# Performance work log

Hardware: AMD Instinct MI355X
Metric: run time of the kernel (lower is better)

Reference implementation:

```python
import jax, jax.numpy as jnp
import numpy as np

DIM = 64        # feature channels of x
HEADS = 4
POS_DIM = 3
NUM_IDS = 8
STR_IN = 512    # strength_linear input size
B, S, W = 4, 1024, 8   # batch, sequence (S1), source-views (S2)


def setup_inputs() -> dict:
    key = jax.random.key(0)
    ks = jax.random.split(key, 18)
    stdv = 1.0 / np.sqrt(DIM * DIM)  # embedding init per module
    d8 = DIM // 8
    u = lambda k, shp, s: jax.random.uniform(k, shp, jnp.float32, -s, s)
    return {
        "x": jax.random.normal(ks[0], (B, DIM, S, W), jnp.float32),
        "pos": jax.random.normal(ks[1], (B, S, POS_DIM), jnp.float32),
        "strength": jax.random.normal(ks[2], (STR_IN,), jnp.float32),
        "embed_id1": 3,
        "q_emb_w": u(ks[3], (NUM_IDS, DIM * DIM), stdv),
        "k_emb_w": u(ks[4], (NUM_IDS, DIM * DIM), stdv),
        "v_emb_w": u(ks[5], (NUM_IDS, DIM * DIM), stdv),
        "pos_w1": u(ks[6], (POS_DIM, POS_DIM), 1.0 / np.sqrt(POS_DIM)),
        "pos_b1": u(ks[7], (POS_DIM,), 1.0 / np.sqrt(POS_DIM)),
        "pos_w2": u(ks[8], (d8, POS_DIM), 1.0 / np.sqrt(POS_DIM)),
        "pos_b2": u(ks[9], (d8,), 1.0 / np.sqrt(POS_DIM)),
        "head_w": u(ks[10], (HEADS, d8), 1.0 / np.sqrt(d8)),
        "head_b": u(ks[11], (HEADS,), 1.0 / np.sqrt(d8)),
        "gate": jnp.ones((HEADS,), jnp.float32),
        "out_w": u(ks[12], (DIM, DIM), 1.0 / np.sqrt(DIM)),
        "out_b": u(ks[13], (DIM,), 1.0 / np.sqrt(DIM)),
        "str_w": u(ks[14], (DIM, STR_IN), 1.0 / np.sqrt(STR_IN)),
        "str_b": u(ks[15], (DIM,), 1.0 / np.sqrt(STR_IN)),
    }


def reference(x, pos, strength, embed_id1, q_emb_w, k_emb_w, v_emb_w,
              pos_w1, pos_b1, pos_w2, pos_b2, head_w, head_b, gate,
              out_w, out_b, str_w, str_b):
    # strength projection: Linear(512, dim)
    s = strength @ str_w.T + str_b                    # [dim]
    xt = jnp.transpose(x, (0, 2, 3, 1))               # [B, S, W, dim]
    qe = q_emb_w[embed_id1].reshape(DIM, DIM)
    ke = k_emb_w[embed_id1].reshape(DIM, DIM)
    ve = v_emb_w[embed_id1].reshape(DIM, DIM)

    def proj(emb):
        y = xt @ emb.T + s                            # [B, S, W, dim]
        # collapse (W, dim) -> (heads, head_dim), heads to axis 1
        y = y.reshape(B, S, HEADS, -1)
        return jnp.transpose(y, (0, 2, 1, 3))         # [B, H, S, hd]

    q, k, v = proj(qe), proj(ke), proj(ve)
    hd = q.shape[-1]
    attn = jax.nn.softmax(jnp.einsum("bhsd,bhtd->bhst", q, k) / np.sqrt(hd), axis=-1)

    # relative-position attention branch
    ph = jax.nn.relu(pos @ pos_w1.T + pos_b1) @ pos_w2.T + pos_b2   # [B, S, dim//8]
    diff = ph[:, :, None, :] - ph[:, None, :, :]                    # [B, S, S, dim//8]
    pos_attn = jnp.transpose(diff @ head_w.T + head_b, (0, 3, 1, 2))
    pos_attn = jax.nn.softmax(pos_attn, axis=-1)                    # [B, H, S, S]

    g = jax.nn.sigmoid(gate).reshape(1, -1, 1, 1)
    attn = (1.0 - g) * attn + g * pos_attn
    attn = attn / jnp.sum(attn, axis=-1, keepdims=True)

    out = jnp.einsum("bhst,bhtd->bhsd", attn, v)      # [B, H, S, hd]
    out = jnp.transpose(out, (0, 2, 1, 3)).reshape(B, S, W, DIM)
    return out @ out_w.T + out_b                      # [B, S, W, dim]
```

## Files before the change

kernel.cpp:

```cpp
#include <hip/hip_runtime.h>
#include <math.h>
#include <stdint.h>

#define B_ 4
#define S_ 1024
#define F_ 512
#define HD 128
#define SOFT_C 4.0f

typedef __attribute__((ext_vector_type(8))) short short8;
typedef __attribute__((ext_vector_type(4))) float f32x4;
typedef __attribute__((ext_vector_type(4))) unsigned int u32x4;
typedef __attribute__((ext_vector_type(2))) unsigned int u32x2;

__device__ __forceinline__ unsigned short f2bf(float f) {
    unsigned int u = __float_as_uint(f);
    u = (u + 0x7FFFu + ((u >> 16) & 1u)) >> 16;
    return (unsigned short)u;
}
__device__ __forceinline__ float bf2f(unsigned int s) {
    return __uint_as_float(s << 16);
}
__device__ __forceinline__ void pack_hilo(const float* v, u32x4& hi, u32x4& lo) {
    #pragma unroll
    for (int p = 0; p < 4; ++p) {
        unsigned int h0 = f2bf(v[2 * p]), h1 = f2bf(v[2 * p + 1]);
        float l0 = v[2 * p] - bf2f(h0), l1 = v[2 * p + 1] - bf2f(h1);
        hi[p] = h0 | (h1 << 16);
        lo[p] = (unsigned int)f2bf(l0) | ((unsigned int)f2bf(l1) << 16);
    }
}

__global__ __launch_bounds__(256) void k_qkv(
    const float* __restrict__ x, const int* __restrict__ embed_id,
    const float* __restrict__ qw, const float* __restrict__ kw,
    const float* __restrict__ vw,
    const float* __restrict__ strength, const float* __restrict__ str_w,
    const float* __restrict__ str_b,
    const float* __restrict__ pos, const float* __restrict__ pw1,
    const float* __restrict__ pb1, const float* __restrict__ pw2,
    const float* __restrict__ pb2, const float* __restrict__ head_w,
    unsigned short* __restrict__ yqh, unsigned short* __restrict__ ykh,
    unsigned short* __restrict__ yvt2,
    float* __restrict__ sv_g, float* __restrict__ xbar)
{
    __shared__ unsigned short whi[3][4096];
    __shared__ unsigned short wlo[3][4096];
    __shared__ float part_s[4][64];
    __shared__ float sv_s[64], svq_s[64];
    __shared__ float xr_s[4][8];
    __shared__ float red_s[4][4];
    __shared__ float inv_s[4];

    const int tid  = threadIdx.x;
    const int wv   = tid >> 6;
    const int lane = tid & 63;
    const int quad = lane >> 4;
    const int l15  = lane & 15;
    const float SCALE = 0.08838834764831845f;

    if (blockIdx.x >= 256) {
        const int bi = blockIdx.x - 256;
        const int b = bi >> 6, c = bi & 63;
        float w1_[9], b1_[3], w2_[24], b2_[8], hw_[32];
        #pragma unroll
        for (int i = 0; i < 9; ++i)  w1_[i] = pw1[i];
        #pragma unroll
        for (int i = 0; i < 3; ++i)  b1_[i] = pb1[i];
        #pragma unroll
        for (int i = 0; i < 24; ++i) w2_[i] = pw2[i];
        #pragma unroll
        for (int i = 0; i < 8; ++i)  b2_[i] = pb2[i];
        #pragma unroll
        for (int i = 0; i < 32; ++i) hw_[i] = head_w[i];

        float pv_[4][4];
        float ps[4] = {0.f, 0.f, 0.f, 0.f};
        #pragma unroll
        for (int rr = 0; rr < 4; ++rr) {
            const int s = tid * 4 + rr;
            float p0 = pos[(b * S_ + s) * 3 + 0];
            float p1 = pos[(b * S_ + s) * 3 + 1];
            float p2 = pos[(b * S_ + s) * 3 + 2];
            float h0 = fmaxf(0.f, p0 * w1_[0] + p1 * w1_[1] + p2 * w1_[2] + b1_[0]);
            float h1 = fmaxf(0.f, p0 * w1_[3] + p1 * w1_[4] + p2 * w1_[5] + b1_[1]);
            float h2 = fmaxf(0.f, p0 * w1_[6] + p1 * w1_[7] + p2 * w1_[8] + b1_[2]);
            float ph[8];
            #pragma unroll
            for (int o8 = 0; o8 < 8; ++o8)
                ph[o8] = h0 * w2_[o8 * 3] + h1 * w2_[o8 * 3 + 1]
                       + h2 * w2_[o8 * 3 + 2] + b2_[o8];
            #pragma unroll
            for (int h = 0; h < 4; ++h) {
                float A = 0.f;
                #pragma unroll
                for (int o8 = 0; o8 < 8; ++o8) A += ph[o8] * hw_[h * 8 + o8];
                pv_[rr][h] = __expf(-A - 1.0f);
                ps[h] += pv_[rr][h];
            }
        }
        #pragma unroll
        for (int h = 0; h < 4; ++h)
            #pragma unroll
            for (int off = 1; off < 64; off <<= 1)
                ps[h] += __shfl_xor(ps[h], off);
        if (lane == 0)
            #pragma unroll
            for (int h = 0; h < 4; ++h) red_s[wv][h] = ps[h];
        __syncthreads();
        if (tid < 4)
            inv_s[tid] = 1.f / (red_s[0][tid] + red_s[1][tid]
                              + red_s[2][tid] + red_s[3][tid]);
        __syncthreads();

        const float* xc = x + (size_t)b * 524288 + c * 8192;
        float acc[8] = {};
        #pragma unroll
        for (int rr = 0; rr < 4; ++rr) {
            const int s = tid * 4 + rr;
            f32x4 x0 = *(const f32x4*)(xc + s * 8);
            f32x4 x1 = *(const f32x4*)(xc + s * 8 + 4);
            float q0 = pv_[rr][0] * inv_s[0];
            float q1 = pv_[rr][1] * inv_s[1];
            float q2 = pv_[rr][2] * inv_s[2];
            float q3 = pv_[rr][3] * inv_s[3];
            acc[0] += q0 * x0[0]; acc[1] += q0 * x0[1];
            acc[2] += q1 * x0[2]; acc[3] += q1 * x0[3];
            acc[4] += q2 * x1[0]; acc[5] += q2 * x1[1];
            acc[6] += q3 * x1[2]; acc[7] += q3 * x1[3];
        }
        #pragma unroll
        for (int j = 0; j < 8; ++j)
            #pragma unroll
            for (int off = 1; off < 64; off <<= 1)
                acc[j] += __shfl_xor(acc[j], off);
        if (lane == 0)
            #pragma unroll
            for (int j = 0; j < 8; ++j) xr_s[wv][j] = acc[j];
        __syncthreads();
        if (tid < 8)
            xbar[(b * 8 + tid) * 64 + c] = xr_s[0][tid] + xr_s[1][tid]
                                         + xr_s[2][tid] + xr_s[3][tid];
        return;
    }

    const int id = embed_id[0];

    for (int cc = tid; cc < 1536; cc += 256) {
        const int m  = cc >> 9;
        const int e0 = (cc & 511) << 3;
        const float* src = (m == 0 ? qw : m == 1 ? kw : vw) + id * 4096 + e0;
        const float sc = (m == 0) ? SCALE : 1.0f;
        f32x4 a0 = *(const f32x4*)src;
        f32x4 a1 = *(const f32x4*)(src + 4);
        float v8[8] = {a0[0] * sc, a0[1] * sc, a0[2] * sc, a0[3] * sc,
                       a1[0] * sc, a1[1] * sc, a1[2] * sc, a1[3] * sc};
        u32x4 hi, lo;
        pack_hilo(v8, hi, lo);
        const int r = e0 >> 6, c = e0 & 63;
        const int off = ((r >> 4) * 2 + (c >> 5)) * 512
                      + ((c >> 3) & 3) * 128 + (r & 15) * 8;
        *(u32x4*)(&whi[m][off]) = hi;
        *(u32x4*)(&wlo[m][off]) = lo;
    }

    {
        const float* wrow = str_w + lane * 512 + wv * 128;
        const float* st   = strength + wv * 128;
        float a = 0.f;
        #pragma unroll
        for (int j4 = 0; j4 < 32; ++j4) {
            f32x4 wv4 = *(const f32x4*)(wrow + j4 * 4);
            f32x4 s4  = *(const f32x4*)(st + j4 * 4);
            a += wv4[0] * s4[0] + wv4[1] * s4[1] + wv4[2] * s4[2] + wv4[3] * s4[3];
        }
        part_s[wv][lane] = a;
    }
    __syncthreads();
    if (tid < 64) {
        float v = part_s[0][tid] + part_s[1][tid] + part_s[2][tid]
                + part_s[3][tid] + str_b[tid];
        sv_s[tid]  = v;
        svq_s[tid] = v * SCALE;
        if (blockIdx.x == 0) sv_g[tid] = v;
    }
    __syncthreads();

    float svq_l[4], sv_l[4];
    #pragma unroll
    for (int nt = 0; nt < 4; ++nt) {
        svq_l[nt] = svq_s[nt * 16 + l15];
        sv_l[nt]  = sv_s[nt * 16 + l15];
    }
    f32x4 svA[4];
    #pragma unroll
    for (int mt = 0; mt < 4; ++mt)
        svA[mt] = *(const f32x4*)&sv_s[mt * 16 + quad * 4];

    #pragma unroll
    for (int u = 0; u < 2; ++u) {
        const int r0   = (blockIdx.x * 2 + u) * 64 + wv * 16;
        const int b    = r0 >> 13;
        const int rloc = (r0 & 8191) + l15;
        const float* xb = x + (size_t)b * 524288;

        u32x4 xhi[2], xlo[2];
        #pragma unroll
        for (int kc = 0; kc < 2; ++kc) {
            float xv[8];
            #pragma unroll
            for (int j = 0; j < 8; ++j)
                xv[j] = xb[(kc * 32 + quad * 8 + j) * 8192 + rloc];
            pack_hilo(xv, xhi[kc], xlo[kc]);
        }

        int idxq[4];
        #pragma unroll
        for (int rr = 0; rr < 4; ++rr) {
            const int rl = quad * 4 + rr;
            const int w_ = rl & 7;
            const int s_loc = ((r0 & 8191) >> 3) + (rl >> 3);
            idxq[rr] = (b * 4 + (w_ >> 1)) * 131072 + s_loc * 128 + (w_ & 1) * 64 + l15;
        }

        const int row_g = r0 + l15;
        const int s_idx = (row_g >> 3) & 1023;
        const int w_idx = row_g & 7;
        const int bh    = b * 4 + (w_idx >> 1);
        const int dbase = (w_idx & 1) * 64;
        unsigned short* vtb = yvt2 + (size_t)bh * 131072 + (s_idx >> 6) * 8192
                            + (size_t)dbase * 64 + (s_idx & 63);

        #pragma unroll
        for (int mat = 0; mat < 2; ++mat) {
            const unsigned short* mh = whi[mat];
            const unsigned short* ml = wlo[mat];
            f32x4 acc[4] = {};
            #pragma unroll
            for (int kc = 0; kc < 2; ++kc)
                #pragma unroll
                for (int nt = 0; nt < 4; ++nt) {
                    const int off = (nt * 2 + kc) * 512 + quad * 128 + l15 * 8;
                    u32x4 ehi = *(const u32x4*)(mh + off);
                    u32x4 elo = *(const u32x4*)(ml + off);
                    acc[nt] = __builtin_amdgcn_mfma_f32_16x16x32_bf16(
                        __builtin_bit_cast(short8, xhi[kc]),
                        __builtin_bit_cast(short8, ehi), acc[nt], 0, 0, 0);
                    acc[nt] = __builtin_amdgcn_mfma_f32_16x16x32_bf16(
                        __builtin_bit_cast(short8, xlo[kc]),
                        __builtin_bit_cast(short8, ehi), acc[nt], 0, 0, 0);
                    acc[nt] = __builtin_amdgcn_mfma_f32_16x16x32_bf16(
                        __builtin_bit_cast(short8, xhi[kc]),
                        __builtin_bit_cast(short8, elo), acc[nt], 0, 0, 0);
                }
            unsigned short* y = (mat == 0 ? yqh : ykh);
            const float* svp = (mat == 0 ? svq_l : sv_l);
            #pragma unroll
            for (int nt = 0; nt < 4; ++nt)
                #pragma unroll
                for (int rr = 0; rr < 4; ++rr)
                    y[(size_t)idxq[rr] + nt * 16] = f2bf(acc[nt][rr] + svp[nt]);
        }

        {
            const unsigned short* mh = whi[2];
            const unsigned short* ml = wlo[2];
            f32x4 acc[4] = {};
            #pragma unroll
            for (int kc = 0; kc < 2; ++kc)
                #pragma unroll
                for (int mt = 0; mt < 4; ++mt) {
                    const int off = (mt * 2 + kc) * 512 + quad * 128 + l15 * 8;
                    u32x4 ehi = *(const u32x4*)(mh + off);
                    u32x4 elo = *(const u32x4*)(ml + off);
                    acc[mt] = __builtin_amdgcn_mfma_f32_16x16x32_bf16(
                        __builtin_bit_cast(short8, ehi),
                        __builtin_bit_cast(short8, xhi[kc]), acc[mt], 0, 0, 0);
                    acc[mt] = __builtin_amdgcn_mfma_f32_16x16x32_bf16(
                        __builtin_bit_cast(short8, ehi),
                        __builtin_bit_cast(short8, xlo[kc]), acc[mt], 0, 0, 0);
                    acc[mt] = __builtin_amdgcn_mfma_f32_16x16x32_bf16(
                        __builtin_bit_cast(short8, elo),
                        __builtin_bit_cast(short8, xhi[kc]), acc[mt], 0, 0, 0);
                }
            #pragma unroll
            for (int mt = 0; mt < 4; ++mt)
                #pragma unroll
                for (int rr = 0; rr < 4; ++rr) {
                    const int c = mt * 16 + quad * 4 + rr;
                    vtb[(size_t)c * 64] = f2bf(acc[mt][rr] + svA[mt][rr]);
                }
        }
    }
}

__global__ __launch_bounds__(256, 2) void k_attn(
    const unsigned short* __restrict__ yqh, const unsigned short* __restrict__ ykh,
    const unsigned short* __restrict__ yvt2,
    const float* __restrict__ xbar, const float* __restrict__ vw,
    const int* __restrict__ embed_id, const float* __restrict__ sv,
    const float* __restrict__ gate,
    const float* __restrict__ out_w, const float* __restrict__ out_b,
    float* __restrict__ out)
{
    __shared__ __align__(16) unsigned short kx[2][64 * 136];
    __shared__ __align__(16) unsigned short vx[2][128 * 72];
    __shared__ float vbar_s[128];
    __shared__ float vbarP_s[128];
    __shared__ float lsq_s[2][2][16];

    const int tid  = threadIdx.x;
    const int w    = tid >> 6;
    const int lane = tid & 63;
    const int quad = lane >> 4;
    const int l15  = lane & 15;
    const int bh = blockIdx.x & 15, qt = blockIdx.x >> 4;
    const int b = bh >> 2, h = bh & 3;
    const int s0 = qt * 32;
    const int qh = w >> 1;
    const int ts = w & 1;

    const unsigned short* ykb = ykh + (size_t)bh * 131072;
    const unsigned short* yvb = yvt2 + (size_t)bh * 131072;

    if (tid < 128) {
        const int c = tid & 63, wloc = tid >> 6;
        const float* ver = vw + embed_id[0] * 4096 + c * 64;
        const float* xbr = xbar + (b * 8 + h * 2 + wloc) * 64;
        float a = sv[c];
        #pragma unroll
        for (int j4 = 0; j4 < 16; ++j4) {
            f32x4 e4 = *(const f32x4*)(ver + j4 * 4);
            f32x4 x4 = *(const f32x4*)(xbr + j4 * 4);
            a += e4[0] * x4[0] + e4[1] * x4[1] + e4[2] * x4[2] + e4[3] * x4[3];
        }
        vbar_s[wloc * 64 + c] = a;
    }

    u32x4 qf[4];
    #pragma unroll
    for (int kc = 0; kc < 4; ++kc)
        qf[kc] = *(const u32x4*)(yqh + (size_t)bh * 131072
                 + (s0 + qh * 16 + l15) * 128 + kc * 32 + quad * 8);

    #pragma unroll
    for (int r = 0; r < 4; ++r) {
        const int off = r * 2048 + tid * 8;
        *(u32x4*)&kx[0][(off >> 7) * 136 + (off & 127)] =
            *(const u32x4*)(ykb + off);
        *(u32x4*)&vx[0][(off >> 6) * 72 + (off & 63)] =
            *(const u32x4*)(yvb + off);
    }
    __syncthreads();

    if (tid < 128) {
        const int seg = tid >> 6, dq = tid & 63;
        const float* wr = out_w + dq * 64;
        float a = 0.f;
        #pragma unroll
        for (int j4 = 0; j4 < 16; ++j4) {
            f32x4 w4 = *(const f32x4*)(wr + j4 * 4);
            f32x4 v4 = *(const f32x4*)&vbar_s[seg * 64 + j4 * 4];
            a += w4[0] * v4[0] + w4[1] * v4[1] + w4[2] * v4[2] + w4[3] * v4[3];
        }
        vbarP_s[seg * 64 + dq] = a;
    }

    f32x4 o[8] = {};
    float lsum = 0.f;
    const int srcA = ((quad & 1) << 5) + l15;

    for (int it = 0; it < 16; ++it) {
        const int cur = it & 1;
        u32x4 kst[4], vst[4];
        const bool pre = (it < 15);
        if (pre) {
            const unsigned short* ksrc = ykb + (it + 1) * 8192;
            const unsigned short* vsrc = yvb + (it + 1) * 8192;
            #pragma unroll
            for (int r = 0; r < 4; ++r)
                kst[r] = *(const u32x4*)(ksrc + r * 2048 + tid * 8);
            #pragma unroll
            for (int r = 0; r < 4; ++r)
                vst[r] = *(const u32x4*)(vsrc + r * 2048 + tid * 8);
        }

        const unsigned short* kxc = kx[cur];
        const unsigned short* vxc = vx[cur];

        f32x4 sa0 = {}, sa1 = {};
        #pragma unroll
        for (int kc = 0; kc < 4; ++kc) {
            u32x4 a0 = *(const u32x4*)&kxc[(ts * 32 + l15) * 136 + kc * 32 + quad * 8];
            sa0 = __builtin_amdgcn_mfma_f32_16x16x32_bf16(
                __builtin_bit_cast(short8, a0),
                __builtin_bit_cast(short8, qf[kc]), sa0, 0, 0, 0);
        }
        #pragma unroll
        for (int kc = 0; kc < 4; ++kc) {
            u32x4 a1 = *(const u32x4*)&kxc[(ts * 32 + 16 + l15) * 136 + kc * 32 + quad * 8];
            sa1 = __builtin_amdgcn_mfma_f32_16x16x32_bf16(
                __builtin_bit_cast(short8, a1),
                __builtin_bit_cast(short8, qf[kc]), sa1, 0, 0, 0);
        }

        float p0[4], p1[4];
        #pragma unroll
        for (int r = 0; r < 4; ++r) {
            p0[r] = __expf(sa0[r] - SOFT_C);
            p1[r] = __expf(sa1[r] - SOFT_C);
            lsum += p0[r] + p1[r];
        }

        unsigned int pk00 = (unsigned int)f2bf(p0[0]) | ((unsigned int)f2bf(p0[1]) << 16);
        unsigned int pk01 = (unsigned int)f2bf(p0[2]) | ((unsigned int)f2bf(p0[3]) << 16);
        unsigned int pk10 = (unsigned int)f2bf(p1[0]) | ((unsigned int)f2bf(p1[1]) << 16);
        unsigned int pk11 = (unsigned int)f2bf(p1[2]) | ((unsigned int)f2bf(p1[3]) << 16);
        unsigned int sel0 = (quad < 2) ? pk00 : pk10;
        unsigned int sel1 = (quad < 2) ? pk01 : pk11;
        u32x4 pf;
        pf[0] = (unsigned int)__shfl((int)sel0, srcA);
        pf[1] = (unsigned int)__shfl((int)sel1, srcA);
        pf[2] = (unsigned int)__shfl((int)sel0, srcA + 16);
        pf[3] = (unsigned int)__shfl((int)sel1, srcA + 16);

        #pragma unroll
        for (int dt = 0; dt < 8; ++dt) {
            u32x4 vf = *(const u32x4*)&vxc[(dt * 16 + l15) * 72 + ts * 32 + quad * 8];
            o[dt] = __builtin_amdgcn_mfma_f32_16x16x32_bf16(
                __builtin_bit_cast(short8, vf),
                __builtin_bit_cast(short8, pf), o[dt], 0, 0, 0);
        }

        if (pre) {
            #pragma unroll
            for (int r = 0; r < 4; ++r) {
                const int off = r * 2048 + tid * 8;
                *(u32x4*)&kx[cur ^ 1][(off >> 7) * 136 + (off & 127)] = kst[r];
            }
            #pragma unroll
            for (int r = 0; r < 4; ++r) {
                const int off = r * 2048 + tid * 8;
                *(u32x4*)&vx[cur ^ 1][(off >> 6) * 72 + (off & 63)] = vst[r];
            }
        }
        __syncthreads();
    }

    float* obuf = (float*)&kx[0][0];
    {
        float* ow_ = obuf + ((qh * 2 + ts) * 16 + l15) * 132;
        #pragma unroll
        for (int dt = 0; dt < 8; ++dt)
            *(f32x4*)(ow_ + dt * 16 + quad * 4) = o[dt];
    }
    lsum += __shfl_xor(lsum, 16);
    lsum += __shfl_xor(lsum, 32);
    if (quad == 0) lsq_s[qh][ts][l15] = lsum;
    __syncthreads();

    const float gf = 1.f / (1.f + __expf(-gate[h]));
    const float cf = (1.f - gf) / (lsq_s[qh][0][l15] + lsq_s[qh][1][l15]);
    const float* oa  = obuf + ((qh * 2 + 0) * 16 + l15) * 132;
    const float* obp = obuf + ((qh * 2 + 1) * 16 + l15) * 132;

    u32x4 bhi[2], blo[2];
    #pragma unroll
    for (int kc = 0; kc < 2; ++kc) {
        const int off = ts * 64 + kc * 32 + quad * 8;
        f32x4 a0 = *(const f32x4*)(oa + off);
        f32x4 a1 = *(const f32x4*)(oa + off + 4);
        f32x4 c0 = *(const f32x4*)(obp + off);
        f32x4 c1 = *(const f32x4*)(obp + off + 4);
        float yv[8] = {cf * (a0[0] + c0[0]), cf * (a0[1] + c0[1]),
                       cf * (a0[2] + c0[2]), cf * (a0[3] + c0[3]),
                       cf * (a1[0] + c1[0]), cf * (a1[1] + c1[1]),
                       cf * (a1[2] + c1[2]), cf * (a1[3] + c1[3])};
        pack_hilo(yv, bhi[kc], blo[kc]);
    }

    f32x4 acc[4] = {};
    #pragma unroll
    for (int kc = 0; kc < 2; ++kc)
        #pragma unroll
        for (int mt = 0; mt < 4; ++mt) {
            const float* wsrc2 = out_w + (mt * 16 + l15) * 64 + kc * 32 + quad * 8;
            f32x4 w0 = *(const f32x4*)wsrc2;
            f32x4 w1 = *(const f32x4*)(wsrc2 + 4);
            float wv8[8] = {w0[0], w0[1], w0[2], w0[3], w1[0], w1[1], w1[2], w1[3]};
            u32x4 ahi, alo;
            pack_hilo(wv8, ahi, alo);
            acc[mt] = __builtin_amdgcn_mfma_f32_16x16x32_bf16(
                __builtin_bit_cast(short8, ahi),
                __builtin_bit_cast(short8, bhi[kc]), acc[mt], 0, 0, 0);
            acc[mt] = __builtin_amdgcn_mfma_f32_16x16x32_bf16(
                __builtin_bit_cast(short8, ahi),
                __builtin_bit_cast(short8, blo[kc]), acc[mt], 0, 0, 0);
            acc[mt] = __builtin_amdgcn_mfma_f32_16x16x32_bf16(
                __builtin_bit_cast(short8, alo),
                __builtin_bit_cast(short8, bhi[kc]), acc[mt], 0, 0, 0);
        }

    const int w_seg = h * 2 + ts;
    const size_t rowb = ((size_t)(b * S_ + s0 + qh * 16 + l15) * 8 + w_seg) * 64;
    #pragma unroll
    for (int mt = 0; mt < 4; ++mt) {
        f32x4 vb   = *(const f32x4*)&vbarP_s[ts * 64 + mt * 16 + quad * 4];
        f32x4 bias = *(const f32x4*)(out_b + mt * 16 + quad * 4);
        f32x4 res;
        #pragma unroll
        for (int j = 0; j < 4; ++j) res[j] = acc[mt][j] + gf * vb[j] + bias[j];
        *(f32x4*)(out + rowb + mt * 16 + quad * 4) = res;
    }
}

extern "C" void kernel_launch(void* const* d_in, const int* in_sizes, int n_in,
                              void* d_out, int out_size, void* d_ws, size_t ws_size,
                              hipStream_t stream) {
    (void)in_sizes; (void)n_in; (void)out_size; (void)ws_size;
    const float* x        = (const float*)d_in[0];
    const float* pos      = (const float*)d_in[1];
    const float* strength = (const float*)d_in[2];
    const int*   embed_id = (const int*)d_in[3];
    const float* qw       = (const float*)d_in[4];
    const float* kw       = (const float*)d_in[5];
    const float* vw       = (const float*)d_in[6];
    const float* pw1      = (const float*)d_in[7];
    const float* pb1      = (const float*)d_in[8];
    const float* pw2      = (const float*)d_in[9];
    const float* pb2      = (const float*)d_in[10];
    const float* head_w   = (const float*)d_in[11];
    const float* gate     = (const float*)d_in[13];
    const float* out_w    = (const float*)d_in[14];
    const float* out_b    = (const float*)d_in[15];
    const float* str_w    = (const float*)d_in[16];
    const float* str_b    = (const float*)d_in[17];
    float* out = (float*)d_out;

    unsigned short* yqh   = (unsigned short*)d_ws;
    unsigned short* ykh   = yqh + 2097152;
    unsigned short* yvt2  = ykh + 2097152;
    float* sv   = (float*)(yvt2 + 2097152);
    float* xbar = sv + 64;

    k_qkv<<<512, 256, 0, stream>>>(x, embed_id, qw, kw, vw,
                                   strength, str_w, str_b,
                                   pos, pw1, pb1, pw2, pb2, head_w,
                                   yqh, ykh, yvt2, sv, xbar);
    k_attn<<<512, 256, 0, stream>>>(yqh, ykh, yvt2, xbar, vw, embed_id, sv,
                                    gate, out_w, out_b, out);
}
```

Before: 141.0 us.

## Load K/V MFMA fragments directly from global into registers, drop LDS staging

Replaces the LDS double-buffered K/V tile staging in the attention kernel with direct per-lane global loads of the MFMA operand fragments into registers, software-pipelined with two register buffers. This removes the LDS writes and reads and the per-iteration __syncthreads. In exchange, each wave fetches K/V separately, so global/L2 traffic rises and register pressure grows (32 extra u32x4 live), which may hurt occupancy under launch_bounds(256,2).

```diff
diff --git a/kernel.cpp b/kernel.cpp
--- a/kernel.cpp
+++ b/kernel.cpp
@@ -303,8 +303,7 @@
     const float* __restrict__ out_w, const float* __restrict__ out_b,
     float* __restrict__ out)
 {
-    __shared__ __align__(16) unsigned short kx[2][64 * 136];
-    __shared__ __align__(16) unsigned short vx[2][128 * 72];
+    __shared__ __align__(16) float obuf[64 * 132];
     __shared__ float vbar_s[128];
     __shared__ float vbarP_s[128];
     __shared__ float lsq_s[2][2][16];
@@ -320,8 +319,10 @@
     const int qh = w >> 1;
     const int ts = w & 1;
 
-    const unsigned short* ykb = ykh + (size_t)bh * 131072;
-    const unsigned short* yvb = yvt2 + (size_t)bh * 131072;
+    const unsigned short* kfb = ykh + (size_t)bh * 131072
+                              + (ts * 32 + l15) * 128 + quad * 8;
+    const unsigned short* vfb = yvt2 + (size_t)bh * 131072
+                              + l15 * 64 + ts * 32 + quad * 8;
 
     if (tid < 128) {
         const int c = tid & 63, wloc = tid >> 6;
@@ -343,14 +344,6 @@
         qf[kc] = *(const u32x4*)(yqh + (size_t)bh * 131072
                  + (s0 + qh * 16 + l15) * 128 + kc * 32 + quad * 8);
 
-    #pragma unroll
-    for (int r = 0; r < 4; ++r) {
-        const int off = r * 2048 + tid * 8;
-        *(u32x4*)&kx[0][(off >> 7) * 136 + (off & 127)] =
-            *(const u32x4*)(ykb + off);
-        *(u32x4*)&vx[0][(off >> 6) * 72 + (off & 63)] =
-            *(const u32x4*)(yvb + off);
-    }
     __syncthreads();
 
     if (tid < 128) {
@@ -370,39 +363,31 @@
     float lsum = 0.f;
     const int srcA = ((quad & 1) << 5) + l15;
 
-    for (int it = 0; it < 16; ++it) {
-        const int cur = it & 1;
-        u32x4 kst[4], vst[4];
-        const bool pre = (it < 15);
-        if (pre) {
-            const unsigned short* ksrc = ykb + (it + 1) * 8192;
-            const unsigned short* vsrc = yvb + (it + 1) * 8192;
-            #pragma unroll
-            for (int r = 0; r < 4; ++r)
-                kst[r] = *(const u32x4*)(ksrc + r * 2048 + tid * 8);
-            #pragma unroll
-            for (int r = 0; r < 4; ++r)
-                vst[r] = *(const u32x4*)(vsrc + r * 2048 + tid * 8);
-        }
-
-        const unsigned short* kxc = kx[cur];
-        const unsigned short* vxc = vx[cur];
-
+    auto loadkv = [&](int it, u32x4* ka, u32x4* vv) {
+        const unsigned short* kt = kfb + it * 8192;
+        #pragma unroll
+        for (int kc = 0; kc < 4; ++kc) {
+            ka[kc]     = *(const u32x4*)(kt + kc * 32);
+            ka[4 + kc] = *(const u32x4*)(kt + 2048 + kc * 32);
+        }
+        const unsigned short* vt = vfb + it * 8192;
+        #pragma unroll
+        for (int dt = 0; dt < 8; ++dt)
+            vv[dt] = *(const u32x4*)(vt + dt * 1024);
+    };
+
+    auto step = [&](const u32x4* ka, const u32x4* vv) {
         f32x4 sa0 = {}, sa1 = {};
         #pragma unroll
-        for (int kc = 0; kc < 4; ++kc) {
-            u32x4 a0 = *(const u32x4*)&kxc[(ts * 32 + l15) * 136 + kc * 32 + quad * 8];
+        for (int kc = 0; kc < 4; ++kc)
             sa0 = __builtin_amdgcn_mfma_f32_16x16x32_bf16(
-                __builtin_bit_cast(short8, a0),
+                __builtin_bit_cast(short8, ka[kc]),
                 __builtin_bit_cast(short8, qf[kc]), sa0, 0, 0, 0);
-        }
-        #pragma unroll
-        for (int kc = 0; kc < 4; ++kc) {
-            u32x4 a1 = *(const u32x4*)&kxc[(ts * 32 + 16 + l15) * 136 + kc * 32 + quad * 8];
+        #pragma unroll
+        for (int kc = 0; kc < 4; ++kc)
             sa1 = __builtin_amdgcn_mfma_f32_16x16x32_bf16(
-                __builtin_bit_cast(short8, a1),
+                __builtin_bit_cast(short8, ka[4 + kc]),
                 __builtin_bit_cast(short8, qf[kc]), sa1, 0, 0, 0);
-        }
 
         float p0[4], p1[4];
         #pragma unroll
@@ -425,29 +410,22 @@
         pf[3] = (unsigned int)__shfl((int)sel1, srcA + 16);
 
         #pragma unroll
-        for (int dt = 0; dt < 8; ++dt) {
-            u32x4 vf = *(const u32x4*)&vxc[(dt * 16 + l15) * 72 + ts * 32 + quad * 8];
+        for (int dt = 0; dt < 8; ++dt)
             o[dt] = __builtin_amdgcn_mfma_f32_16x16x32_bf16(
-                __builtin_bit_cast(short8, vf),
+                __builtin_bit_cast(short8, vv[dt]),
                 __builtin_bit_cast(short8, pf), o[dt], 0, 0, 0);
-        }
-
-        if (pre) {
-            #pragma unroll
-            for (int r = 0; r < 4; ++r) {
-                const int off = r * 2048 + tid * 8;
-                *(u32x4*)&kx[cur ^ 1][(off >> 7) * 136 + (off & 127)] = kst[r];
-            }
-            #pragma unroll
-            for (int r = 0; r < 4; ++r) {
-                const int off = r * 2048 + tid * 8;
-                *(u32x4*)&vx[cur ^ 1][(off >> 6) * 72 + (off & 63)] = vst[r];
-            }
-        }
-        __syncthreads();
-    }
-
-    float* obuf = (float*)&kx[0][0];
+    };
+
+    u32x4 kaA[8], vvA[8], kaB[8], vvB[8];
+    loadkv(0, kaA, vvA);
+    for (int it2 = 0; it2 < 8; ++it2) {
+        const int itA = it2 * 2;
+        loadkv(itA + 1, kaB, vvB);
+        step(kaA, vvA);
+        if (itA + 2 < 16) loadkv(itA + 2, kaA, vvA);
+        step(kaB, vvB);
+    }
+
     {
         float* ow_ = obuf + ((qh * 2 + ts) * 16 + l15) * 132;
         #pragma unroll
```

New measurement: 180.8 us. 1.28x slower.

## Double query tile per attention block to share K/V staging across 8 waves

Applied to the files above, without the earlier changes.

Changes k_attn to launch 256 blocks of 512 threads, each covering 64 queries in two wave groups that share one double-buffered K/V tile in shared memory. Each K/V tile is loaded once per 64 queries instead of once per 32, halving global K/V traffic and per-thread staging loads. In exchange, shared memory use grows (the output scratch buffer must now hold 8 waves' results), there are half as many blocks to spread across CUs, and barriers now synchronize 8 waves.

```diff
diff --git a/kernel.cpp b/kernel.cpp
--- a/kernel.cpp
+++ b/kernel.cpp
@@ -294,7 +294,7 @@
     }
 }
 
-__global__ __launch_bounds__(256, 2) void k_attn(
+__global__ __launch_bounds__(512, 2) void k_attn(
     const unsigned short* __restrict__ yqh, const unsigned short* __restrict__ ykh,
     const unsigned short* __restrict__ yvt2,
     const float* __restrict__ xbar, const float* __restrict__ vw,
@@ -303,11 +303,13 @@
     const float* __restrict__ out_w, const float* __restrict__ out_b,
     float* __restrict__ out)
 {
-    __shared__ __align__(16) unsigned short kx[2][64 * 136];
-    __shared__ __align__(16) unsigned short vx[2][128 * 72];
+    __shared__ __align__(16) unsigned char smem_kv[71680];
     __shared__ float vbar_s[128];
     __shared__ float vbarP_s[128];
-    __shared__ float lsq_s[2][2][16];
+    __shared__ float lsq_s[2][2][2][16];
+
+    unsigned short* kxb = (unsigned short*)smem_kv;
+    unsigned short* vxb = (unsigned short*)(smem_kv + 34816);
 
     const int tid  = threadIdx.x;
     const int w    = tid >> 6;
@@ -316,9 +318,11 @@
     const int l15  = lane & 15;
     const int bh = blockIdx.x & 15, qt = blockIdx.x >> 4;
     const int b = bh >> 2, h = bh & 3;
-    const int s0 = qt * 32;
-    const int qh = w >> 1;
-    const int ts = w & 1;
+    const int g  = w >> 2;
+    const int wl = w & 3;
+    const int qh = wl >> 1;
+    const int ts = wl & 1;
+    const int s0 = qt * 64 + g * 32;
 
     const unsigned short* ykb = ykh + (size_t)bh * 131072;
     const unsigned short* yvb = yvt2 + (size_t)bh * 131072;
@@ -344,11 +348,11 @@
                  + (s0 + qh * 16 + l15) * 128 + kc * 32 + quad * 8);
 
     #pragma unroll
-    for (int r = 0; r < 4; ++r) {
-        const int off = r * 2048 + tid * 8;
-        *(u32x4*)&kx[0][(off >> 7) * 136 + (off & 127)] =
+    for (int r = 0; r < 2; ++r) {
+        const int off = r * 4096 + tid * 8;
+        *(u32x4*)&kxb[(off >> 7) * 136 + (off & 127)] =
             *(const u32x4*)(ykb + off);
-        *(u32x4*)&vx[0][(off >> 6) * 72 + (off & 63)] =
+        *(u32x4*)&vxb[(off >> 6) * 72 + (off & 63)] =
             *(const u32x4*)(yvb + off);
     }
     __syncthreads();
@@ -372,21 +376,21 @@
 
     for (int it = 0; it < 16; ++it) {
         const int cur = it & 1;
-        u32x4 kst[4], vst[4];
+        u32x4 kst[2], vst[2];
         const bool pre = (it < 15);
         if (pre) {
             const unsigned short* ksrc = ykb + (it + 1) * 8192;
             const unsigned short* vsrc = yvb + (it + 1) * 8192;
             #pragma unroll
-            for (int r = 0; r < 4; ++r)
-                kst[r] = *(const u32x4*)(ksrc + r * 2048 + tid * 8);
-            #pragma unroll
-            for (int r = 0; r < 4; ++r)
-                vst[r] = *(const u32x4*)(vsrc + r * 2048 + tid * 8);
-        }
-
-        const unsigned short* kxc = kx[cur];
-        const unsigned short* vxc = vx[cur];
+            for (int r = 0; r < 2; ++r)
+                kst[r] = *(const u32x4*)(ksrc + r * 4096 + tid * 8);
+            #pragma unroll
+            for (int r = 0; r < 2; ++r)
+                vst[r] = *(const u32x4*)(vsrc + r * 4096 + tid * 8);
+        }
+
+        const unsigned short* kxc = kxb + cur * 8704;
+        const unsigned short* vxc = vxb + cur * 9216;
 
         f32x4 sa0 = {}, sa1 = {};
         #pragma unroll
@@ -433,36 +437,38 @@
         }
 
         if (pre) {
-            #pragma unroll
-            for (int r = 0; r < 4; ++r) {
-                const int off = r * 2048 + tid * 8;
-                *(u32x4*)&kx[cur ^ 1][(off >> 7) * 136 + (off & 127)] = kst[r];
+            unsigned short* kxn = kxb + (cur ^ 1) * 8704;
+            unsigned short* vxn = vxb + (cur ^ 1) * 9216;
+            #pragma unroll
+            for (int r = 0; r < 2; ++r) {
+                const int off = r * 4096 + tid * 8;
+                *(u32x4*)&kxn[(off >> 7) * 136 + (off & 127)] = kst[r];
             }
             #pragma unroll
-            for (int r = 0; r < 4; ++r) {
-                const int off = r * 2048 + tid * 8;
-                *(u32x4*)&vx[cur ^ 1][(off >> 6) * 72 + (off & 63)] = vst[r];
+            for (int r = 0; r < 2; ++r) {
+                const int off = r * 4096 + tid * 8;
+                *(u32x4*)&vxn[(off >> 6) * 72 + (off & 63)] = vst[r];
             }
         }
         __syncthreads();
     }
 
-    float* obuf = (float*)&kx[0][0];
+    float* obuf = (float*)smem_kv;
     {
-        float* ow_ = obuf + ((qh * 2 + ts) * 16 + l15) * 132;
+        float* ow_ = obuf + ((g * 4 + qh * 2 + ts) * 16 + l15) * 132;
         #pragma unroll
         for (int dt = 0; dt < 8; ++dt)
             *(f32x4*)(ow_ + dt * 16 + quad * 4) = o[dt];
     }
     lsum += __shfl_xor(lsum, 16);
     lsum += __shfl_xor(lsum, 32);
-    if (quad == 0) lsq_s[qh][ts][l15] = lsum;
+    if (quad == 0) lsq_s[g][qh][ts][l15] = lsum;
     __syncthreads();
 
     const float gf = 1.f / (1.f + __expf(-gate[h]));
-    const float cf = (1.f - gf) / (lsq_s[qh][0][l15] + lsq_s[qh][1][l15]);
-    const float* oa  = obuf + ((qh * 2 + 0) * 16 + l15) * 132;
-    const float* obp = obuf + ((qh * 2 + 1) * 16 + l15) * 132;
+    const float cf = (1.f - gf) / (lsq_s[g][qh][0][l15] + lsq_s[g][qh][1][l15]);
+    const float* oa  = obuf + ((g * 4 + qh * 2 + 0) * 16 + l15) * 132;
+    const float* obp = obuf + ((g * 4 + qh * 2 + 1) * 16 + l15) * 132;
 
     u32x4 bhi[2], blo[2];
     #pragma unroll
@@ -547,6 +553,6 @@
                                    strength, str_w, str_b,
                                    pos, pw1, pb1, pw2, pb2, head_w,
                                    yqh, ykh, yvt2, sv, xbar);
-    k_attn<<<512, 256, 0, stream>>>(yqh, ykh, yvt2, xbar, vw, embed_id, sv,
+    k_attn<<<256, 512, 0, stream>>>(yqh, ykh, yvt2, xbar, vw, embed_id, sv,
                                     gate, out_w, out_b, out);
 }
```

Result: faster. 137.8 us (-2.3%).
